# Optimization experiments

Measured on AMD Instinct MI355X. Metric: run time of the kernel, lower is better.

Reference implementation:

```python
import jax, jax.numpy as jnp
import numpy as np

N_NODES = 10000
NUM_FEAT = 128
HIDD = 256
HEADS = 8
NUM_CLASS = 10
NEG_SLOPE = 0.2


def _gat_conv(x, src, dst, W, att_src, att_dst, bias, n_nodes):
    # x: [N, F_in]; W: [F_in, H*C]; att_*: [H, C]; bias: [H*C]
    H, C = att_src.shape
    h = (x @ W).reshape(n_nodes, H, C)                      # [N, H, C]
    a_src = jnp.einsum('nhc,hc->nh', h, att_src)            # [N, H]
    a_dst = jnp.einsum('nhc,hc->nh', h, att_dst)            # [N, H]
    e = a_src[src] + a_dst[dst]                             # [E, H]
    e = jnp.where(e >= 0, e, NEG_SLOPE * e)                 # leaky_relu
    # segment softmax over edges grouped by destination node
    e_max = jax.ops.segment_max(jax.lax.stop_gradient(e), dst, num_segments=n_nodes)
    e_max = jnp.where(jnp.isfinite(e_max), e_max, 0.0)
    ex = jnp.exp(e - e_max[dst])                            # [E, H]
    denom = jax.ops.segment_sum(ex, dst, num_segments=n_nodes)
    alpha = ex / (denom[dst] + 1e-16)                       # [E, H]
    msg = h[src] * alpha[:, :, None]                        # [E, H, C]
    out = jax.ops.segment_sum(msg, dst, num_segments=n_nodes)
    return out.reshape(n_nodes, H * C) + bias


def setup_inputs() -> dict:
    key = jax.random.key(0)
    ks = jax.random.split(key, 12)
    x = jax.random.normal(ks[0], (N_NODES, NUM_FEAT), dtype=jnp.float32)
    edge_index = jax.random.randint(ks[1], (2, 50000), 0, N_NODES, dtype=jnp.int64)
    g1 = 1.0 / np.sqrt(NUM_FEAT)
    g2 = 1.0 / np.sqrt(HEADS * HIDD)
    return {
        'x': x,
        'edge_index': edge_index,
        'W1': jax.random.normal(ks[2], (NUM_FEAT, HEADS * HIDD), dtype=jnp.float32) * g1,
        'att_src1': jax.random.normal(ks[3], (HEADS, HIDD), dtype=jnp.float32) * g2,
        'att_dst1': jax.random.normal(ks[4], (HEADS, HIDD), dtype=jnp.float32) * g2,
        'b1': jnp.zeros((HEADS * HIDD,), dtype=jnp.float32),
        'W2': jax.random.normal(ks[5], (HEADS * HIDD, NUM_CLASS), dtype=jnp.float32) * g2,
        'att_src2': jax.random.normal(ks[6], (1, NUM_CLASS), dtype=jnp.float32),
        'att_dst2': jax.random.normal(ks[7], (1, NUM_CLASS), dtype=jnp.float32),
        'b2': jnp.zeros((NUM_CLASS,), dtype=jnp.float32),
    }


def reference(x, edge_index, W1, att_src1, att_dst1, b1, W2, att_src2, att_dst2, b2):
    n = x.shape[0]
    # PyG GATConv default add_self_loops=True
    loop = jnp.arange(n, dtype=edge_index.dtype)
    src = jnp.concatenate([edge_index[0], loop])
    dst = jnp.concatenate([edge_index[1], loop])
    h = _gat_conv(x, src, dst, W1, att_src1, att_dst1, b1, n)
    h = jax.nn.elu(h)
    h = _gat_conv(h, src, dst, W2, att_src2, att_dst2, b2, n)
    return jax.nn.sigmoid(h)
```

## Files before the change

kernel.cpp:

```cpp
#include <hip/hip_runtime.h>
#include <math.h>

#define N_NODES 10000
#define N_PAD   10112
#define E0      50000
#define E_TOT   60000
#define FIN     128
#define HEADS   8
#define CHN     256
#define HC      2048
#define NC      10
#define NEG     0.2f
#define MAXD    128
#define MAXD2   64

typedef __attribute__((ext_vector_type(8))) short bf16x8;
typedef __attribute__((ext_vector_type(4))) float f32x4;

__device__ __forceinline__ unsigned f2u(float f){
  unsigned u = __float_as_uint(f);
  return (u & 0x80000000u) ? ~u : (u | 0x80000000u);
}
__device__ __forceinline__ float u2f(unsigned u){
  return __uint_as_float((u & 0x80000000u) ? (u & 0x7fffffffu) : ~u);
}
__device__ __forceinline__ unsigned short bf16_rne(float f){
  unsigned u = __float_as_uint(f);
  return (unsigned short)((u + 0x7FFFu + ((u >> 16) & 1u)) >> 16);
}

__global__ void k_init(const int* __restrict__ raw, int* __restrict__ flag,
                       int* __restrict__ deg, int* __restrict__ cursor){
  int t = blockIdx.x*256 + threadIdx.x;
  if (t < N_NODES){ deg[t] = 0; cursor[t] = 0; }
  if (blockIdx.x == 0 && threadIdx.x < 64){
    int i = threadIdx.x;
    bool bad = (raw[2*i + 1] != 0) || ((unsigned)raw[2*i] >= (unsigned)N_NODES);
    unsigned long long b = __ballot(bad);
    if (i == 0) *flag = (b == 0ull) ? 1 : 0;
  }
}

__global__ void k_convert(const int* __restrict__ raw, const int* __restrict__ flag,
                          int* __restrict__ esrc, int* __restrict__ edst,
                          int* __restrict__ deg){
  int e = blockIdx.x * blockDim.x + threadIdx.x;
  if (e >= E_TOT) return;
  int s, d;
  if (e < E0){
    if (*flag){ s = raw[2*e]; d = raw[2*(E0 + e)]; }
    else      { s = raw[e];   d = raw[E0 + e];     }
  } else {
    s = d = e - E0;
  }
  esrc[e] = s; edst[e] = d;
  atomicAdd(&deg[d], 1);
}

__global__ __launch_bounds__(256) void k_prepw(const float* __restrict__ W1,
                                               const float* __restrict__ att_src,
                                               const float* __restrict__ att_dst,
                                               const float* __restrict__ W2,
                                               unsigned short* __restrict__ w1t_hi,
                                               unsigned short* __restrict__ w1t_lo,
                                               float* __restrict__ W2t,
                                               float* __restrict__ vv){
  int t = blockIdx.x*256 + threadIdx.x;
  {
    int k = t >> 11;
    int n = t & 2047;
    float v = W1[(size_t)k*HC + n];
    unsigned short hi = bf16_rne(v);
    float hf = __uint_as_float((unsigned)hi << 16);
    unsigned short lo = bf16_rne(v - hf);
    w1t_hi[(size_t)n*FIN + k] = hi;
    w1t_lo[(size_t)n*FIN + k] = lo;
  }
  if (t < HC*NC){
    int j = t >> 11, k = t & 2047;
    W2t[(size_t)j*HC + k] = W2[(size_t)k*NC + j];
  }
  if (t < FIN*HEADS){
    int k = t >> 3, h = t & 7;
    const float* wrow = W1 + (size_t)k*HC + h*CHN;
    const float* as   = att_src + h*CHN;
    const float* ad   = att_dst + h*CHN;
    float s = 0.f, d = 0.f;
    #pragma unroll 4
    for (int c = 0; c < CHN; c += 4){
      float4 w = *reinterpret_cast<const float4*>(wrow + c);
      float4 a = *reinterpret_cast<const float4*>(as + c);
      float4 b = *reinterpret_cast<const float4*>(ad + c);
      s += w.x*a.x + w.y*a.y + w.z*a.z + w.w*a.w;
      d += w.x*b.x + w.y*b.y + w.z*b.z + w.w*b.w;
    }
    vv[k*16 + h]     = s;
    vv[k*16 + 8 + h] = d;
  }
}

__global__ __launch_bounds__(256) void k_attdot(const float* __restrict__ x,
                                                const float* __restrict__ vv,
                                                float* __restrict__ a_src,
                                                float* __restrict__ a_dst){
  const int wave = threadIdx.x >> 6, lane = threadIdx.x & 63;
  const int n = blockIdx.x*4 + wave;
  const int u = lane & 15, c = lane >> 4;
  const float* xr = x + (size_t)n*FIN + c*32;
  float acc = 0.f;
  #pragma unroll
  for (int q = 0; q < 8; ++q){
    float4 xv = *reinterpret_cast<const float4*>(xr + q*4);
    int k = c*32 + q*4;
    acc = fmaf(xv.x, vv[(k+0)*16 + u], acc);
    acc = fmaf(xv.y, vv[(k+1)*16 + u], acc);
    acc = fmaf(xv.z, vv[(k+2)*16 + u], acc);
    acc = fmaf(xv.w, vv[(k+3)*16 + u], acc);
  }
  acc += __shfl_xor(acc, 16);
  acc += __shfl_xor(acc, 32);
  if (c == 0){
    if (u < 8) a_src[n*HEADS + u] = acc;
    else       a_dst[n*HEADS + (u - 8)] = acc;
  }
}

__global__ __launch_bounds__(1024) void k_scan(const int* __restrict__ deg,
                                               int* __restrict__ offs){
  __shared__ int sums[1024];
  const int tid = threadIdx.x;
  int base = tid*10;
  int vals[10];
  int local = 0;
  #pragma unroll
  for (int i = 0; i < 10; ++i){
    int idx = base + i;
    int v = (idx < N_NODES) ? deg[idx] : 0;
    vals[i] = local;
    local += v;
  }
  sums[tid] = local;
  __syncthreads();
  for (int o = 1; o < 1024; o <<= 1){
    int t = (tid >= o) ? sums[tid - o] : 0;
    __syncthreads();
    sums[tid] += t;
    __syncthreads();
  }
  int boff = (tid == 0) ? 0 : sums[tid - 1];
  #pragma unroll
  for (int i = 0; i < 10; ++i){
    int idx = base + i;
    if (idx < N_NODES) offs[idx] = boff + vals[i];
  }
  if (tid == 1023) offs[N_NODES] = sums[1023];
}

__global__ void k_scatter(const int* __restrict__ esrc, const int* __restrict__ edst,
                          const int* __restrict__ offs, int* __restrict__ cursor,
                          int* __restrict__ csr_src){
  int e = blockIdx.x*256 + threadIdx.x;
  if (e < E_TOT){
    int d = edst[e];
    int pos = offs[d] + atomicAdd(&cursor[d], 1);
    csr_src[pos] = esrc[e];
  }
}

__global__ __launch_bounds__(128) void k_aggx(const float* __restrict__ x,
                                              const float* __restrict__ a_src1,
                                              const float* __restrict__ a_dst1,
                                              const int* __restrict__ offs,
                                              const int* __restrict__ csr_src,
                                              unsigned short* __restrict__ agg_hi,
                                              unsigned short* __restrict__ agg_lo){
  __shared__ float s_e[MAXD][HEADS];
  __shared__ int s_src[MAXD];
  __shared__ unsigned s_maxu[HEADS];
  __shared__ float s_sum[HEADS];
  __shared__ float s_inv[HEADS];
  __shared__ float s_ad[HEADS];
  const int n = blockIdx.x, tid = threadIdx.x;
  const int start = offs[n];
  int deg = offs[n+1] - start;
  if (deg > MAXD) deg = MAXD;
  if (tid < HEADS){
    s_maxu[tid] = 0u;
    s_sum[tid] = 0.f;
    s_ad[tid] = a_dst1[n*HEADS + tid];
  }
  for (int i = tid; i < deg; i += 128) s_src[i] = csr_src[start + i];
  __syncthreads();
  const int tot = deg*HEADS;
  for (int i = tid; i < tot; i += 128){
    int e = i >> 3, hh = i & 7;
    float v = a_src1[s_src[e]*HEADS + hh] + s_ad[hh];
    v = (v >= 0.f) ? v : NEG*v;
    s_e[e][hh] = v;
    atomicMax(&s_maxu[hh], f2u(v));
  }
  __syncthreads();
  for (int i = tid; i < tot; i += 128){
    int e = i >> 3, hh = i & 7;
    float v = expf(s_e[e][hh] - u2f(s_maxu[hh]));
    s_e[e][hh] = v;
    atomicAdd(&s_sum[hh], v);
  }
  __syncthreads();
  if (tid < HEADS) s_inv[tid] = 1.f/(s_sum[tid] + 1e-16f);
  __syncthreads();
  for (int i = tid; i < tot; i += 128) s_e[i>>3][i&7] *= s_inv[i&7];
  __syncthreads();
  float acc[HEADS] = {0,0,0,0,0,0,0,0};
  for (int e = 0; e < deg; ++e){
    float xv = x[(size_t)s_src[e]*FIN + tid];
    #pragma unroll
    for (int h = 0; h < HEADS; ++h) acc[h] = fmaf(s_e[e][h], xv, acc[h]);
  }
  #pragma unroll
  for (int h = 0; h < HEADS; ++h){
    float v = acc[h];
    unsigned short hi = bf16_rne(v);
    float hf = __uint_as_float((unsigned)hi << 16);
    unsigned short lo = bf16_rne(v - hf);
    size_t idx = ((size_t)n*HEADS + h)*FIN + tid;
    agg_hi[idx] = hi;
    agg_lo[idx] = lo;
  }
}

__global__ __launch_bounds__(256) void k_gemm1(const unsigned short* __restrict__ agg_hi,
                                               const unsigned short* __restrict__ agg_lo,
                                               const unsigned short* __restrict__ w1t_hi,
                                               const unsigned short* __restrict__ w1t_lo,
                                               const float* __restrict__ b1,
                                               float* __restrict__ out1){
  const int tid = threadIdx.x;
  const int bx = blockIdx.x;
  const int by = blockIdx.y;
  const int h  = bx >> 1;
  const int colbase = bx*128;
  const int wave = tid >> 6, lane = tid & 63;
  const int wr = wave >> 1, wc = wave & 1;
  const int nl = lane & 15, g = lane >> 4;

  f32x4 zero4 = {0.f, 0.f, 0.f, 0.f};
  f32x4 acc[4][4];
  #pragma unroll
  for (int fm = 0; fm < 4; ++fm)
    #pragma unroll
    for (int fn = 0; fn < 4; ++fn) acc[fm][fn] = zero4;

  const size_t abase = (((size_t)(by*128 + wr*64 + nl))*HEADS + h)*FIN + g*8;
  const size_t bbase = ((size_t)(colbase + wc*64 + nl))*FIN + g*8;

  #pragma unroll
  for (int kc = 0; kc < 4; ++kc){
    bf16x8 ah[4], al[4], bh[4], bl[4];
    #pragma unroll
    for (int f = 0; f < 4; ++f){
      size_t ao = abase + (size_t)f*16*HEADS*FIN + kc*32;
      size_t bo = bbase + (size_t)f*16*FIN + kc*32;
      ah[f] = *reinterpret_cast<const bf16x8*>(agg_hi + ao);
      al[f] = *reinterpret_cast<const bf16x8*>(agg_lo + ao);
      bh[f] = *reinterpret_cast<const bf16x8*>(w1t_hi + bo);
      bl[f] = *reinterpret_cast<const bf16x8*>(w1t_lo + bo);
    }
    #pragma unroll
    for (int fm = 0; fm < 4; ++fm)
      #pragma unroll
      for (int fn = 0; fn < 4; ++fn){
        acc[fm][fn] = __builtin_amdgcn_mfma_f32_16x16x32_bf16(ah[fm], bh[fn], acc[fm][fn], 0, 0, 0);
        acc[fm][fn] = __builtin_amdgcn_mfma_f32_16x16x32_bf16(ah[fm], bl[fn], acc[fm][fn], 0, 0, 0);
        acc[fm][fn] = __builtin_amdgcn_mfma_f32_16x16x32_bf16(al[fm], bh[fn], acc[fm][fn], 0, 0, 0);
      }
  }

  #pragma unroll
  for (int fm = 0; fm < 4; ++fm){
    #pragma unroll
    for (int fn = 0; fn < 4; ++fn){
      int col = colbase + wc*64 + fn*16 + nl;
      float bb = b1[col];
      #pragma unroll
      for (int r = 0; r < 4; ++r){
        int row = by*128 + wr*64 + fm*16 + g*4 + r;
        if (row < N_NODES){
          float v = acc[fm][fn][r] + bb;
          v = (v > 0.f) ? v : (__expf(v) - 1.f);
          out1[(size_t)row*HC + col] = v;
        }
      }
    }
  }
}

__global__ __launch_bounds__(256) void k_gemv2(const float* __restrict__ out1,
                                               const float* __restrict__ W2t,
                                               const float* __restrict__ as2,
                                               const float* __restrict__ ad2,
                                               float* __restrict__ h2,
                                               float* __restrict__ a_src2,
                                               float* __restrict__ a_dst2){
  const int tid = threadIdx.x;
  const int nl = tid & 15;
  const int ng = tid >> 4;
  const int n = blockIdx.x*16 + ng;
  float acc[NC];
  #pragma unroll
  for (int j = 0; j < NC; ++j) acc[j] = 0.f;
  const float* row = out1 + (size_t)n*HC;
  for (int i = 0; i < 32; ++i){
    int k = i*64 + nl*4;
    float4 v = *reinterpret_cast<const float4*>(row + k);
    #pragma unroll
    for (int j = 0; j < NC; ++j){
      float4 w = *reinterpret_cast<const float4*>(W2t + (size_t)j*HC + k);
      acc[j] += v.x*w.x + v.y*w.y + v.z*w.z + v.w*w.w;
    }
  }
  #pragma unroll
  for (int o = 1; o < 16; o <<= 1){
    #pragma unroll
    for (int j = 0; j < NC; ++j) acc[j] += __shfl_xor(acc[j], o);
  }
  if (nl == 0){
    float ds = 0.f, dd = 0.f;
    #pragma unroll
    for (int j = 0; j < NC; ++j){
      h2[(size_t)n*NC + j] = acc[j];
      ds = fmaf(acc[j], as2[j], ds);
      dd = fmaf(acc[j], ad2[j], dd);
    }
    a_src2[n] = ds;
    a_dst2[n] = dd;
  }
}

__global__ __launch_bounds__(64) void k_agg2(const float* __restrict__ h2,
                                             const float* __restrict__ a_src2,
                                             const float* __restrict__ a_dst2,
                                             const int* __restrict__ offs,
                                             const int* __restrict__ csr_src,
                                             const float* __restrict__ b2,
                                             float* __restrict__ out){
  __shared__ float s_al[MAXD2];
  __shared__ int s_sc[MAXD2];
  const int n = blockIdx.x, lane = threadIdx.x;
  const int start = offs[n];
  int deg = offs[n+1] - start;
  if (deg > MAXD2) deg = MAXD2;
  const float ad = a_dst2[n];
  float e = -INFINITY;
  if (lane < deg){
    int src = csr_src[start + lane];
    s_sc[lane] = src;
    e = a_src2[src] + ad;
    e = (e >= 0.f) ? e : NEG*e;
  }
  float m = e;
  #pragma unroll
  for (int o = 1; o < 64; o <<= 1) m = fmaxf(m, __shfl_xor(m, o));
  float ex = (lane < deg) ? expf(e - m) : 0.f;
  float s = ex;
  #pragma unroll
  for (int o = 1; o < 64; o <<= 1) s += __shfl_xor(s, o);
  if (lane < deg) s_al[lane] = ex / (s + 1e-16f);
  __syncthreads();
  if (lane < NC){
    float acc = 0.f;
    for (int i = 0; i < deg; ++i)
      acc = fmaf(s_al[i], h2[(size_t)s_sc[i]*NC + lane], acc);
    float v = acc + b2[lane];
    out[n*NC + lane] = 1.f/(1.f + expf(-v));
  }
}

extern "C" void kernel_launch(void* const* d_in, const int* in_sizes, int n_in,
                              void* d_out, int out_size, void* d_ws, size_t ws_size,
                              hipStream_t stream){
  const float* x   = (const float*)d_in[0];
  const int*   ei  = (const int*)  d_in[1];
  const float* W1  = (const float*)d_in[2];
  const float* as1 = (const float*)d_in[3];
  const float* ad1 = (const float*)d_in[4];
  const float* b1  = (const float*)d_in[5];
  const float* W2  = (const float*)d_in[6];
  const float* as2 = (const float*)d_in[7];
  const float* ad2 = (const float*)d_in[8];
  const float* b2  = (const float*)d_in[9];
  float* out = (float*)d_out;

  char* ws = (char*)d_ws;
  size_t off = 0;
  auto alloc = [&](size_t bytes) -> void* {
    void* p = ws + off;
    off += (bytes + 255) & ~(size_t)255;
    return p;
  };
  float* out1    = (float*)alloc((size_t)N_NODES*HC*4);
  unsigned short* agg_hi = (unsigned short*)alloc((size_t)N_PAD*HEADS*FIN*2);
  unsigned short* agg_lo = (unsigned short*)alloc((size_t)N_PAD*HEADS*FIN*2);
  unsigned short* w1t_hi = (unsigned short*)alloc((size_t)HC*FIN*2);
  unsigned short* w1t_lo = (unsigned short*)alloc((size_t)HC*FIN*2);
  float* W2t     = (float*)alloc((size_t)NC*HC*4);
  float* vv      = (float*)alloc((size_t)FIN*16*4);
  float* a_src1  = (float*)alloc((size_t)N_NODES*HEADS*4);
  float* a_dst1  = (float*)alloc((size_t)N_NODES*HEADS*4);
  float* h2      = (float*)alloc((size_t)N_NODES*NC*4);
  float* a_src2  = (float*)alloc((size_t)N_NODES*4);
  float* a_dst2  = (float*)alloc((size_t)N_NODES*4);
  int*   deg     = (int*)alloc((size_t)N_NODES*4);
  int*   offs    = (int*)alloc((size_t)(N_NODES+1)*4);
  int*   cursor  = (int*)alloc((size_t)N_NODES*4);
  int*   esrc    = (int*)alloc((size_t)E_TOT*4);
  int*   edst    = (int*)alloc((size_t)E_TOT*4);
  int*   csr_src = (int*)alloc((size_t)E_TOT*4);
  int*   flag    = (int*)alloc(4);
  (void)ws_size; (void)in_sizes; (void)n_in; (void)out_size;

  k_init   <<<40, 256, 0, stream>>>(ei, flag, deg, cursor);
  k_convert<<<(E_TOT + 255)/256, 256, 0, stream>>>(ei, flag, esrc, edst, deg);
  k_prepw  <<<(HC*FIN)/256, 256, 0, stream>>>(W1, as1, ad1, W2, w1t_hi, w1t_lo, W2t, vv);
  k_attdot <<<N_NODES/4, 256, 0, stream>>>(x, vv, a_src1, a_dst1);
  k_scan   <<<1, 1024, 0, stream>>>(deg, offs);
  k_scatter<<<(E_TOT + 255)/256, 256, 0, stream>>>(esrc, edst, offs, cursor, csr_src);
  k_aggx   <<<N_NODES, 128, 0, stream>>>(x, a_src1, a_dst1, offs, csr_src, agg_hi, agg_lo);
  k_gemm1  <<<dim3(16, N_PAD/128), 256, 0, stream>>>(agg_hi, agg_lo, w1t_hi, w1t_lo, b1, out1);
  k_gemv2  <<<N_NODES/16, 256, 0, stream>>>(out1, W2t, as2, ad2, h2, a_src2, a_dst2);
  k_agg2   <<<N_NODES, 64, 0, stream>>>(h2, a_src2, a_dst2, offs, csr_src, b2, out);
}
```

Measured before the change: 243.7 us.

## Stage GEMM1 A tiles in LDS with head-major layout; tile W2 in shared memory

```diff
diff --git a/kernel.cpp b/kernel.cpp
--- a/kernel.cpp
+++ b/kernel.cpp
@@ -13,6 +13,7 @@
 #define NEG     0.2f
 #define MAXD    128
 #define MAXD2   64
+#define LDSTR   80
 
 typedef __attribute__((ext_vector_type(8))) short bf16x8;
 typedef __attribute__((ext_vector_type(4))) float f32x4;
@@ -60,10 +61,8 @@
 __global__ __launch_bounds__(256) void k_prepw(const float* __restrict__ W1,
                                                const float* __restrict__ att_src,
                                                const float* __restrict__ att_dst,
-                                               const float* __restrict__ W2,
                                                unsigned short* __restrict__ w1t_hi,
                                                unsigned short* __restrict__ w1t_lo,
-                                               float* __restrict__ W2t,
                                                float* __restrict__ vv){
   int t = blockIdx.x*256 + threadIdx.x;
   {
@@ -75,10 +74,6 @@
     unsigned short lo = bf16_rne(v - hf);
     w1t_hi[(size_t)n*FIN + k] = hi;
     w1t_lo[(size_t)n*FIN + k] = lo;
-  }
-  if (t < HC*NC){
-    int j = t >> 11, k = t & 2047;
-    W2t[(size_t)j*HC + k] = W2[(size_t)k*NC + j];
   }
   if (t < FIN*HEADS){
     int k = t >> 3, h = t & 7;
@@ -223,26 +218,32 @@
     unsigned short hi = bf16_rne(v);
     float hf = __uint_as_float((unsigned)hi << 16);
     unsigned short lo = bf16_rne(v - hf);
-    size_t idx = ((size_t)n*HEADS + h)*FIN + tid;
+    size_t idx = ((size_t)h*N_PAD + n)*FIN + tid;
     agg_hi[idx] = hi;
     agg_lo[idx] = lo;
   }
 }
 
-__global__ __launch_bounds__(256) void k_gemm1(const unsigned short* __restrict__ agg_hi,
-                                               const unsigned short* __restrict__ agg_lo,
-                                               const unsigned short* __restrict__ w1t_hi,
-                                               const unsigned short* __restrict__ w1t_lo,
-                                               const float* __restrict__ b1,
-                                               float* __restrict__ out1){
+__global__ __launch_bounds__(256, 4) void k_gemm1(const unsigned short* __restrict__ agg_hi,
+                                                  const unsigned short* __restrict__ agg_lo,
+                                                  const unsigned short* __restrict__ w1t_hi,
+                                                  const unsigned short* __restrict__ w1t_lo,
+                                                  const float* __restrict__ b1,
+                                                  float* __restrict__ out1){
+  __shared__ unsigned short Ahi[128*LDSTR];
+  __shared__ unsigned short Alo[128*LDSTR];
   const int tid = threadIdx.x;
   const int bx = blockIdx.x;
   const int by = blockIdx.y;
   const int h  = bx >> 1;
   const int colbase = bx*128;
+  const int n0 = by*128;
   const int wave = tid >> 6, lane = tid & 63;
   const int wr = wave >> 1, wc = wave & 1;
   const int nl = lane & 15, g = lane >> 4;
+  const int colb = colbase + wc*64;
+
+  const size_t plane = (size_t)h*N_PAD*FIN;
 
   f32x4 zero4 = {0.f, 0.f, 0.f, 0.f};
   f32x4 acc[4][4];
@@ -251,40 +252,52 @@
     #pragma unroll
     for (int fn = 0; fn < 4; ++fn) acc[fm][fn] = zero4;
 
-  const size_t abase = (((size_t)(by*128 + wr*64 + nl))*HEADS + h)*FIN + g*8;
-  const size_t bbase = ((size_t)(colbase + wc*64 + nl))*FIN + g*8;
-
-  #pragma unroll
-  for (int kc = 0; kc < 4; ++kc){
-    bf16x8 ah[4], al[4], bh[4], bl[4];
-    #pragma unroll
-    for (int f = 0; f < 4; ++f){
-      size_t ao = abase + (size_t)f*16*HEADS*FIN + kc*32;
-      size_t bo = bbase + (size_t)f*16*FIN + kc*32;
-      ah[f] = *reinterpret_cast<const bf16x8*>(agg_hi + ao);
-      al[f] = *reinterpret_cast<const bf16x8*>(agg_lo + ao);
-      bh[f] = *reinterpret_cast<const bf16x8*>(w1t_hi + bo);
-      bl[f] = *reinterpret_cast<const bf16x8*>(w1t_lo + bo);
-    }
-    #pragma unroll
-    for (int fm = 0; fm < 4; ++fm)
+  #pragma unroll
+  for (int ch = 0; ch < 2; ++ch){
+    if (ch) __syncthreads();
+    #pragma unroll
+    for (int i = 0; i < 4; ++i){
+      int cid = tid + 256*i;
+      int row = cid >> 3, part = cid & 7;
+      size_t gsrc = plane + (size_t)(n0 + row)*FIN + ch*64 + part*8;
+      int ldst = row*LDSTR + part*8;
+      *reinterpret_cast<bf16x8*>(&Ahi[ldst]) = *reinterpret_cast<const bf16x8*>(agg_hi + gsrc);
+      *reinterpret_cast<bf16x8*>(&Alo[ldst]) = *reinterpret_cast<const bf16x8*>(agg_lo + gsrc);
+    }
+    __syncthreads();
+    #pragma unroll
+    for (int s = 0; s < 2; ++s){
+      bf16x8 ah[4], al[4];
+      #pragma unroll
+      for (int fm = 0; fm < 4; ++fm){
+        int lsrc = (wr*64 + fm*16 + nl)*LDSTR + s*32 + g*8;
+        ah[fm] = *reinterpret_cast<const bf16x8*>(&Ahi[lsrc]);
+        al[fm] = *reinterpret_cast<const bf16x8*>(&Alo[lsrc]);
+      }
       #pragma unroll
       for (int fn = 0; fn < 4; ++fn){
-        acc[fm][fn] = __builtin_amdgcn_mfma_f32_16x16x32_bf16(ah[fm], bh[fn], acc[fm][fn], 0, 0, 0);
-        acc[fm][fn] = __builtin_amdgcn_mfma_f32_16x16x32_bf16(ah[fm], bl[fn], acc[fm][fn], 0, 0, 0);
-        acc[fm][fn] = __builtin_amdgcn_mfma_f32_16x16x32_bf16(al[fm], bh[fn], acc[fm][fn], 0, 0, 0);
+        size_t bo = ((size_t)(colb + fn*16 + nl))*FIN + ch*64 + s*32 + g*8;
+        bf16x8 bh = *reinterpret_cast<const bf16x8*>(w1t_hi + bo);
+        bf16x8 bl = *reinterpret_cast<const bf16x8*>(w1t_lo + bo);
+        #pragma unroll
+        for (int fm = 0; fm < 4; ++fm){
+          acc[fm][fn] = __builtin_amdgcn_mfma_f32_16x16x32_bf16(ah[fm], bh, acc[fm][fn], 0, 0, 0);
+          acc[fm][fn] = __builtin_amdgcn_mfma_f32_16x16x32_bf16(ah[fm], bl, acc[fm][fn], 0, 0, 0);
+          acc[fm][fn] = __builtin_amdgcn_mfma_f32_16x16x32_bf16(al[fm], bh, acc[fm][fn], 0, 0, 0);
+        }
       }
+    }
   }
 
   #pragma unroll
   for (int fm = 0; fm < 4; ++fm){
     #pragma unroll
     for (int fn = 0; fn < 4; ++fn){
-      int col = colbase + wc*64 + fn*16 + nl;
+      int col = colb + fn*16 + nl;
       float bb = b1[col];
       #pragma unroll
       for (int r = 0; r < 4; ++r){
-        int row = by*128 + wr*64 + fm*16 + g*4 + r;
+        int row = n0 + wr*64 + fm*16 + g*4 + r;
         if (row < N_NODES){
           float v = acc[fm][fn][r] + bb;
           v = (v > 0.f) ? v : (__expf(v) - 1.f);
@@ -296,12 +309,13 @@
 }
 
 __global__ __launch_bounds__(256) void k_gemv2(const float* __restrict__ out1,
-                                               const float* __restrict__ W2t,
+                                               const float* __restrict__ W2,
                                                const float* __restrict__ as2,
                                                const float* __restrict__ ad2,
                                                float* __restrict__ h2,
                                                float* __restrict__ a_src2,
                                                float* __restrict__ a_dst2){
+  __shared__ float W2s[256][13];
   const int tid = threadIdx.x;
   const int nl = tid & 15;
   const int ng = tid >> 4;
@@ -310,13 +324,30 @@
   #pragma unroll
   for (int j = 0; j < NC; ++j) acc[j] = 0.f;
   const float* row = out1 + (size_t)n*HC;
-  for (int i = 0; i < 32; ++i){
-    int k = i*64 + nl*4;
-    float4 v = *reinterpret_cast<const float4*>(row + k);
-    #pragma unroll
-    for (int j = 0; j < NC; ++j){
-      float4 w = *reinterpret_cast<const float4*>(W2t + (size_t)j*HC + k);
-      acc[j] += v.x*w.x + v.y*w.y + v.z*w.z + v.w*w.w;
+  for (int c = 0; c < 8; ++c){
+    if (c) __syncthreads();
+    {
+      const float2* src = reinterpret_cast<const float2*>(W2 + (size_t)(c*256 + tid)*NC);
+      #pragma unroll
+      for (int q = 0; q < 5; ++q){
+        float2 w = src[q];
+        W2s[tid][2*q]   = w.x;
+        W2s[tid][2*q+1] = w.y;
+      }
+    }
+    __syncthreads();
+    #pragma unroll
+    for (int i = 0; i < 4; ++i){
+      int kq = i*64 + nl*4;
+      float4 v = *reinterpret_cast<const float4*>(row + c*256 + kq);
+      float vm[4] = {v.x, v.y, v.z, v.w};
+      #pragma unroll
+      for (int m = 0; m < 4; ++m){
+        const float* wrow = &W2s[kq + m][0];
+        #pragma unroll
+        for (int j = 0; j < NC; ++j)
+          acc[j] = fmaf(vm[m], wrow[j], acc[j]);
+      }
     }
   }
   #pragma unroll
@@ -399,11 +430,10 @@
     return p;
   };
   float* out1    = (float*)alloc((size_t)N_NODES*HC*4);
-  unsigned short* agg_hi = (unsigned short*)alloc((size_t)N_PAD*HEADS*FIN*2);
-  unsigned short* agg_lo = (unsigned short*)alloc((size_t)N_PAD*HEADS*FIN*2);
+  unsigned short* agg_hi = (unsigned short*)alloc((size_t)HEADS*N_PAD*FIN*2);
+  unsigned short* agg_lo = (unsigned short*)alloc((size_t)HEADS*N_PAD*FIN*2);
   unsigned short* w1t_hi = (unsigned short*)alloc((size_t)HC*FIN*2);
   unsigned short* w1t_lo = (unsigned short*)alloc((size_t)HC*FIN*2);
-  float* W2t     = (float*)alloc((size_t)NC*HC*4);
   float* vv      = (float*)alloc((size_t)FIN*16*4);
   float* a_src1  = (float*)alloc((size_t)N_NODES*HEADS*4);
   float* a_dst1  = (float*)alloc((size_t)N_NODES*HEADS*4);
@@ -421,12 +451,12 @@
 
   k_init   <<<40, 256, 0, stream>>>(ei, flag, deg, cursor);
   k_convert<<<(E_TOT + 255)/256, 256, 0, stream>>>(ei, flag, esrc, edst, deg);
-  k_prepw  <<<(HC*FIN)/256, 256, 0, stream>>>(W1, as1, ad1, W2, w1t_hi, w1t_lo, W2t, vv);
+  k_prepw  <<<(HC*FIN)/256, 256, 0, stream>>>(W1, as1, ad1, w1t_hi, w1t_lo, vv);
   k_attdot <<<N_NODES/4, 256, 0, stream>>>(x, vv, a_src1, a_dst1);
   k_scan   <<<1, 1024, 0, stream>>>(deg, offs);
   k_scatter<<<(E_TOT + 255)/256, 256, 0, stream>>>(esrc, edst, offs, cursor, csr_src);
   k_aggx   <<<N_NODES, 128, 0, stream>>>(x, a_src1, a_dst1, offs, csr_src, agg_hi, agg_lo);
   k_gemm1  <<<dim3(16, N_PAD/128), 256, 0, stream>>>(agg_hi, agg_lo, w1t_hi, w1t_lo, b1, out1);
-  k_gemv2  <<<N_NODES/16, 256, 0, stream>>>(out1, W2t, as2, ad2, h2, a_src2, a_dst2);
+  k_gemv2  <<<N_NODES/16, 256, 0, stream>>>(out1, W2, as2, ad2, h2, a_src2, a_dst2);
   k_agg2   <<<N_NODES, 64, 0, stream>>>(h2, a_src2, a_dst2, offs, csr_src, b2, out);
 }
```

After: 244.4 us. No clear change (+0.3%).
